# Performance work log

Hardware: AMD Instinct MI355X
Metric: run time of the kernel (lower is better)

The kernel has to match this reference:

```python
import jax, jax.numpy as jnp
import numpy as np

N_HEADS = 4
NS_STEPS = 5
NS_EPS = 1e-7

def newtonschulz5(G):
    # G: [out, in]; quintic Newton-Schulz, 5 steps. out==in here so no transpose branch needed,
    # but keep the static-shape check for faithfulness.
    a, b, c = 3.4445, -4.775, 2.0315
    X = G / (jnp.linalg.norm(G) + NS_EPS)
    transposed = G.shape[0] > G.shape[1]
    if transposed:
        X = X.T
    def step(X, _):
        A = X @ X.T
        B = b * A + c * (A @ A)
        return a * X + B @ X, None
    X, _ = jax.lax.scan(step, X, None, length=NS_STEPS)
    if transposed:
        X = X.T
    return X

def setup_inputs() -> dict:
    key = jax.random.key(0)
    k1, k2, k3, k4, k5 = jax.random.split(key, 5)
    B, S, D_in, D_out, r = 4, 2048, 4096, 4096, 16
    init_std = 0.01 / np.sqrt(D_out * r)
    return {
        "x": jax.random.normal(k1, (B, S, D_in), dtype=jnp.float32),
        "W": jax.random.normal(k2, (D_out, D_in), dtype=jnp.float32) * 0.02,
        "bias": jax.random.normal(k3, (D_out,), dtype=jnp.float32) * 0.02,
        "lora_A": jax.random.normal(k4, (r, D_in), dtype=jnp.float32),
        "lora_B": jax.random.normal(k5, (D_out, r), dtype=jnp.float32) * init_std,
    }

def reference(x, W, bias, lora_A, lora_B):
    # base linear (frozen weights); dropout is identity (p=0 / eval)
    base_out = jnp.einsum('bsi,oi->bso', x, W) + bias
    r, D_in = lora_A.shape
    D_out = lora_B.shape[0]
    hr = r // N_HEADS
    Ah = lora_A.reshape(N_HEADS, hr, D_in)                       # [h, hr, in]
    Bh = lora_B.reshape(D_out, N_HEADS, hr).transpose(1, 0, 2)    # [h, out, hr]
    G = jnp.einsum('hor,hri->hoi', Bh, Ah)                        # [h, out, in]
    alpha = jnp.sqrt(jnp.sum(G * G, axis=(1, 2)))                 # per-head Frobenius norm
    M = jax.vmap(newtonschulz5)(G)                                # [h, out, in]
    lora_out = jnp.einsum('h,hoi,bsi->bso', alpha, M, x)
    return base_out + lora_out
```

## Files before the change

### kernel.cpp

```cpp
#include <hip/hip_runtime.h>
#include <math.h>

#define MDIM 8192
#define NDIM 4096
#define KDIM 4096

typedef __attribute__((ext_vector_type(8))) _Float16 h8;
typedef __attribute__((ext_vector_type(4))) _Float16 h4;
typedef __attribute__((ext_vector_type(4))) float f32x4;

typedef const __attribute__((address_space(1))) void* gas_ptr;
typedef __attribute__((address_space(3))) void* las_ptr;

__device__ inline void load16_to_lds(const void* g, void* l) {
  __builtin_amdgcn_global_load_lds((gas_ptr)g, (las_ptr)l, 16, 0, 0);
}

__device__ inline void mm4(const double* A, const double* B, double* C) {
#pragma unroll
  for (int p = 0; p < 4; ++p)
#pragma unroll
    for (int q = 0; q < 4; ++q) {
      double s = 0.0;
#pragma unroll
      for (int r = 0; r < 4; ++r) s += A[p * 4 + r] * B[r * 4 + q];
      C[p * 4 + q] = s;
    }
}
__device__ inline void mm4_bt(const double* A, const double* B, double* C) {
#pragma unroll
  for (int p = 0; p < 4; ++p)
#pragma unroll
    for (int q = 0; q < 4; ++q) {
      double s = 0.0;
#pragma unroll
      for (int r = 0; r < 4; ++r) s += A[p * 4 + r] * B[q * 4 + r];
      C[p * 4 + q] = s;
    }
}

__global__ void ns_kernel(const float* __restrict__ lora_A,
                          const float* __restrict__ lora_B,
                          float* __restrict__ E) {
  const int h = blockIdx.x;
  const int tid = threadIdx.x;
  const int lane = tid & 63;
  const int wave = tid >> 6;

  float gu[16], gv[16];
#pragma unroll
  for (int e = 0; e < 16; ++e) { gu[e] = 0.f; gv[e] = 0.f; }

  for (int o = tid; o < NDIM; o += 256) {
    const float4 bv = *(const float4*)(lora_B + (size_t)o * 16 + h * 4);
    const float bb[4] = {bv.x, bv.y, bv.z, bv.w};
#pragma unroll
    for (int p = 0; p < 4; ++p)
#pragma unroll
      for (int q = 0; q < 4; ++q) gu[p * 4 + q] += bb[p] * bb[q];
  }
  for (int i = tid; i < KDIM; i += 256) {
    float aa[4];
#pragma unroll
    for (int p = 0; p < 4; ++p) aa[p] = lora_A[(size_t)(h * 4 + p) * KDIM + i];
#pragma unroll
    for (int p = 0; p < 4; ++p)
#pragma unroll
      for (int q = 0; q < 4; ++q) gv[p * 4 + q] += aa[p] * aa[q];
  }

#pragma unroll
  for (int e = 0; e < 16; ++e) {
#pragma unroll
    for (int off = 32; off > 0; off >>= 1) {
      gu[e] += __shfl_down(gu[e], off, 64);
      gv[e] += __shfl_down(gv[e], off, 64);
    }
  }
  __shared__ float pu[4][16], pv[4][16];
  if (lane == 0) {
#pragma unroll
    for (int e = 0; e < 16; ++e) { pu[wave][e] = gu[e]; pv[wave][e] = gv[e]; }
  }
  __syncthreads();

  if (tid == 0) {
    double gud[16], gvd[16];
#pragma unroll
    for (int e = 0; e < 16; ++e) {
      gud[e] = (double)pu[0][e] + pu[1][e] + pu[2][e] + pu[3][e];
      gvd[e] = (double)pv[0][e] + pv[1][e] + pv[2][e] + pv[3][e];
    }
    double tr = 0.0;
#pragma unroll
    for (int e = 0; e < 16; ++e) tr += gud[e] * gvd[e];
    const double alpha = sqrt(tr);
    const double n0 = alpha + 1e-7;

    double C[16] = {0};
    C[0] = C[5] = C[10] = C[15] = 1.0 / n0;

    const double a = 3.4445, b = -4.775, c = 2.0315;
    for (int it = 0; it < 5; ++it) {
      double T1[16], D[16], DG[16], DGD[16], GuC[16], F[16], Cn[16];
      mm4(C, gvd, T1);
      mm4_bt(T1, C, D);
      mm4(D, gud, DG);
      mm4(DG, D, DGD);
      mm4(gud, C, GuC);
#pragma unroll
      for (int e = 0; e < 16; ++e) F[e] = b * D[e] + c * DGD[e];
      mm4(F, GuC, Cn);
#pragma unroll
      for (int e = 0; e < 16; ++e) C[e] = a * C[e] + Cn[e];
    }
#pragma unroll
    for (int e = 0; e < 16; ++e) E[h * 16 + e] = (float)(alpha * C[e]);
  }
}

__global__ void weff_kernel(const float* __restrict__ W,
                            const float* __restrict__ lora_A,
                            const float* __restrict__ lora_B,
                            const float* __restrict__ E,
                            _Float16* __restrict__ Wh) {
  const int tid = threadIdx.x;
  __shared__ float cf[16][16];
  __shared__ __align__(16) float Asm[16][1024];
  const int o0 = (blockIdx.x >> 1) * 16;
  const int kh = (blockIdx.x & 1) * 2048;
  {
    const int r = tid >> 4, kk = tid & 15, h = kk >> 2, q = kk & 3;
    float s = 0.f;
#pragma unroll
    for (int p = 0; p < 4; ++p)
      s += lora_B[(size_t)(o0 + r) * 16 + h * 4 + p] * E[h * 16 + p * 4 + q];
    cf[r][kk] = s;
  }
  for (int kb = kh; kb < kh + 2048; kb += 1024) {
    __syncthreads();
#pragma unroll
    for (int j = 0; j < 16; ++j) {
      const int f4 = tid + j * 256;
      const int k = f4 >> 8, c4 = f4 & 255;
      *(float4*)&Asm[k][c4 * 4] =
          *(const float4*)&lora_A[(size_t)k * KDIM + kb + (size_t)c4 * 4];
    }
    __syncthreads();
    float4 av[16];
#pragma unroll
    for (int k = 0; k < 16; ++k) av[k] = *(const float4*)&Asm[k][tid * 4];
#pragma unroll
    for (int r = 0; r < 16; ++r) {
      const size_t base = (size_t)(o0 + r) * KDIM + kb + tid * 4;
      float4 acc = *(const float4*)&W[base];
#pragma unroll
      for (int k = 0; k < 16; ++k) {
        const float cfv = cf[r][k];
        acc.x += cfv * av[k].x; acc.y += cfv * av[k].y;
        acc.z += cfv * av[k].z; acc.w += cfv * av[k].w;
      }
      h4 pk;
      pk[0] = (_Float16)acc.x; pk[1] = (_Float16)acc.y;
      pk[2] = (_Float16)acc.z; pk[3] = (_Float16)acc.w;
      *(h4*)(Wh + base) = pk;
    }
  }
}

__global__ void xcast_kernel(const float* __restrict__ x,
                             _Float16* __restrict__ Xh) {
  const size_t t = (size_t)blockIdx.x * 256 + threadIdx.x;
  const size_t base = t * 8;
  const float4 a = *(const float4*)(x + base);
  const float4 b = *(const float4*)(x + base + 4);
  h8 o;
  o[0] = (_Float16)a.x; o[1] = (_Float16)a.y; o[2] = (_Float16)a.z; o[3] = (_Float16)a.w;
  o[4] = (_Float16)b.x; o[5] = (_Float16)b.y; o[6] = (_Float16)b.z; o[7] = (_Float16)b.w;
  *(h8*)(Xh + base) = o;
}

__launch_bounds__(512, 2)
__global__ void gemm_kernel(const _Float16* __restrict__ Xh,
                            const _Float16* __restrict__ Wh,
                            const float* __restrict__ bias,
                            float* __restrict__ out) {
  __shared__ __align__(16) _Float16 sA0_0[128 * 64], sA0_1[128 * 64];
  __shared__ __align__(16) _Float16 sA1_0[128 * 64], sA1_1[128 * 64];
  __shared__ __align__(16) _Float16 sB0_0[128 * 64], sB0_1[128 * 64];
  __shared__ __align__(16) _Float16 sB1_0[128 * 64], sB1_1[128 * 64];

  const int tid = threadIdx.x;
  const int lane = tid & 63;
  const int wave = tid >> 6;
  const int wm = wave >> 2;
  const int wn = wave & 3;
  const int quad = lane >> 4;
  const int r16 = lane & 15;
  const int sw = r16 & 7;

  const int lin = blockIdx.x;
  const int wg = (lin & 7) * 64 + (lin >> 3);
  const int bm = wg >> 4;
  const int bn = wg & 15;

  const int row0 = tid >> 3;
  const int lc0 = (tid & 7) ^ (row0 & 7);
  const size_t off0 = (size_t)row0 * KDIM + lc0 * 8;
  const int ldsb = tid * 16;
  const _Float16* pA0 = Xh + (size_t)(bm * 256) * KDIM;
  const _Float16* pA1 = pA0 + (size_t)128 * KDIM;
  const _Float16* pB0 = Wh + (size_t)(bn * 256) * KDIM;
  const _Float16* pB1 = pB0 + (size_t)128 * KDIM;

  const int aRow = (wm * 64 + r16) * 64;
  const int bRow = (wn * 32 + r16) * 64;
  const int c0 = (quad ^ sw) * 8;
  const int c1 = ((quad + 4) ^ sw) * 8;

  f32x4 acc[2][2][4][2] = {};
  h8 a0[4][2], a1[4][2], b0[2][2], b1[2][2];

#define STAGE(arr, p, koff) do {                                               \
    load16_to_lds((p) + off0 + (koff), (char*)(arr) + ldsb);                   \
    load16_to_lds((p) + off0 + (size_t)64 * KDIM + (koff),                     \
                  (char*)(arr) + ldsb + 8192);                                 \
  } while (0)

#define FENCE() asm volatile("" ::: "memory")
#define BAR() do { FENCE(); __builtin_amdgcn_s_barrier(); FENCE(); } while (0)
#define VMC(n) asm volatile("s_waitcnt vmcnt(" #n ")" ::: "memory")

#define RDA(dst, Aarr) do { _Pragma("unroll")                                  \
    for (int f = 0; f < 4; ++f) {                                              \
      dst[f][0] = *(const h8*)&Aarr[aRow + f * 1024 + c0];                     \
      dst[f][1] = *(const h8*)&Aarr[aRow + f * 1024 + c1];                     \
    } } while (0)
#define RDB(dst, Barr) do { _Pragma("unroll")                                  \
    for (int g = 0; g < 2; ++g) {                                              \
      dst[g][0] = *(const h8*)&Barr[bRow + g * 1024 + c0];                     \
      dst[g][1] = *(const h8*)&Barr[bRow + g * 1024 + c1];                     \
    } } while (0)

#define MFMA16(MQ, NQ, AV, BV) do {                                            \
    __builtin_amdgcn_s_setprio(1);                                             \
    _Pragma("unroll")                                                          \
    for (int f = 0; f < 4; ++f)                                                \
      _Pragma("unroll")                                                        \
      for (int g = 0; g < 2; ++g) {                                            \
        acc[MQ][NQ][f][g] = __builtin_amdgcn_mfma_f32_16x16x32_f16(            \
            AV[f][0], BV[g][0], acc[MQ][NQ][f][g], 0, 0, 0);                   \
        acc[MQ][NQ][f][g] = __builtin_amdgcn_mfma_f32_16x16x32_f16(            \
            AV[f][1], BV[g][1], acc[MQ][NQ][f][g], 0, 0, 0);                   \
      }                                                                        \
    __builtin_amdgcn_s_setprio(0);                                             \
  } while (0)

#define NOP() do { } while (0)

#define PH(RDS, STG, MQ, NQ, AV, BV, VMW) do {                                 \
    RDS;                                                                       \
    STG;                                                                       \
    BAR();                                                                     \
    MFMA16(MQ, NQ, AV, BV);                                                    \
    VMW;                                                                       \
    BAR();                                                                     \
  } while (0)

#define TILE_EVEN(t) do {                                                      \
    PH({ RDA(a0, sA0_0); RDB(b0, sB0_0); },                                    \
       STAGE(sA0_1, pA0, ((t) + 1) * 64), 0, 0, a0, b0, VMC(6));               \
    PH(RDA(a1, sA1_0), STAGE(sB1_1, pB1, ((t) + 1) * 64), 1, 0, a1, b0, VMC(6)); \
    PH(RDB(b1, sB1_0), STAGE(sB0_0, pB0, ((t) + 2) * 64), 1, 1, a1, b1, VMC(6)); \
    PH(NOP(),          STAGE(sA1_0, pA1, ((t) + 2) * 64), 0, 1, a0, b1, VMC(6)); \
  } while (0)

#define TILE_ODD(t) do {                                                       \
    PH({ RDA(a0, sA0_1); RDB(b0, sB0_1); },                                    \
       STAGE(sA0_0, pA0, ((t) + 1) * 64), 0, 0, a0, b0, VMC(6));               \
    PH(RDA(a1, sA1_1), STAGE(sB1_0, pB1, ((t) + 1) * 64), 1, 0, a1, b0, VMC(6)); \
    PH(RDB(b1, sB1_1), STAGE(sB0_1, pB0, ((t) + 2) * 64), 1, 1, a1, b1, VMC(6)); \
    PH(NOP(),          STAGE(sA1_1, pA1, ((t) + 2) * 64), 0, 1, a0, b1, VMC(6)); \
  } while (0)

#define TILE_62() do {                                                         \
    PH({ RDA(a0, sA0_0); RDB(b0, sB0_0); },                                    \
       STAGE(sA0_1, pA0, 63 * 64), 0, 0, a0, b0, VMC(6));                      \
    PH(RDA(a1, sA1_0), STAGE(sB1_1, pB1, 63 * 64), 1, 0, a1, b0, VMC(6));      \
    PH(RDB(b1, sB1_0), NOP(), 1, 1, a1, b1, VMC(4));                           \
    PH(NOP(),          NOP(), 0, 1, a0, b1, VMC(2));                           \
  } while (0)

#define TILE_63() do {                                                         \
    PH({ RDA(a0, sA0_1); RDB(b0, sB0_1); }, NOP(), 0, 0, a0, b0, VMC(0));      \
    PH(RDA(a1, sA1_1), NOP(), 1, 0, a1, b0, NOP());                            \
    PH(RDB(b1, sB1_1), NOP(), 1, 1, a1, b1, NOP());                            \
    PH(NOP(),          NOP(), 0, 1, a0, b1, NOP());                            \
  } while (0)

  STAGE(sB0_0, pB0, 0);
  STAGE(sA1_0, pA1, 0);
  STAGE(sA0_0, pA0, 0);
  STAGE(sB1_0, pB1, 0);
  STAGE(sB0_1, pB0, 64);
  STAGE(sA1_1, pA1, 64);
  VMC(4);
  BAR();

#pragma unroll 1
  for (int t2 = 0; t2 < 62; t2 += 2) {
    TILE_EVEN(t2);
    TILE_ODD(t2 + 1);
  }
  TILE_62();
  TILE_63();

#pragma unroll
  for (int mq = 0; mq < 2; ++mq)
#pragma unroll
    for (int f = 0; f < 4; ++f) {
      float* po = out + (size_t)(bm * 256 + mq * 128 + wm * 64 + f * 16 + quad * 4) * NDIM;
#pragma unroll
      for (int nq = 0; nq < 2; ++nq)
#pragma unroll
        for (int g = 0; g < 2; ++g) {
          const int ocol = bn * 256 + nq * 128 + wn * 32 + g * 16 + r16;
          const float bb = bias[ocol];
          const f32x4 v = acc[mq][nq][f][g];
#pragma unroll
          for (int rg = 0; rg < 4; ++rg)
            po[(size_t)rg * NDIM + ocol] = v[rg] + bb;
        }
    }
}

extern "C" void kernel_launch(void* const* d_in, const int* in_sizes, int n_in,
                              void* d_out, int out_size, void* d_ws, size_t ws_size,
                              hipStream_t stream) {
  const float* x      = (const float*)d_in[0];
  const float* W      = (const float*)d_in[1];
  const float* bias   = (const float*)d_in[2];
  const float* lora_A = (const float*)d_in[3];
  const float* lora_B = (const float*)d_in[4];
  float* out = (float*)d_out;

  char* ws = (char*)d_ws;
  float* E = (float*)ws;
  _Float16* Wh = (_Float16*)(ws + 1024);
  _Float16* Xh = (_Float16*)(ws + 1024 + (size_t)NDIM * KDIM * 2);

  ns_kernel<<<dim3(4), dim3(256), 0, stream>>>(lora_A, lora_B, E);
  xcast_kernel<<<dim3((MDIM * KDIM) / (256 * 8)), dim3(256), 0, stream>>>(x, Xh);
  weff_kernel<<<dim3(512), dim3(256), 0, stream>>>(W, lora_A, lora_B, E, Wh);
  gemm_kernel<<<dim3(512), dim3(512), 0, stream>>>(Xh, Wh, bias, out);
}
```

Before: 583.5 us.

## Restructure GEMM to 256x128 tiles with 4 waves and triple-buffered K=32 stages

Replaces the 256x256 block tile with 8 waves and double buffering at K=64 by a 256x128 tile with 4 waves. The K loop now steps by 32 through a three-deep LDS ring. Each wave computes a 128x64 sub-tile with a larger register accumulator, and the grid doubles to 1024 blocks. The goal is more pipeline depth and better per-wave operand reuse. The cost is lower arithmetic intensity per block, more global traffic, and more barriers per unit of work.

```diff
diff --git a/kernel.cpp b/kernel.cpp
--- a/kernel.cpp
+++ b/kernel.cpp
@@ -180,157 +180,125 @@
   *(h8*)(Xh + base) = o;
 }
 
-__launch_bounds__(512, 2)
+__launch_bounds__(256, 2)
 __global__ void gemm_kernel(const _Float16* __restrict__ Xh,
                             const _Float16* __restrict__ Wh,
                             const float* __restrict__ bias,
                             float* __restrict__ out) {
-  __shared__ __align__(16) _Float16 sA0_0[128 * 64], sA0_1[128 * 64];
-  __shared__ __align__(16) _Float16 sA1_0[128 * 64], sA1_1[128 * 64];
-  __shared__ __align__(16) _Float16 sB0_0[128 * 64], sB0_1[128 * 64];
-  __shared__ __align__(16) _Float16 sB1_0[128 * 64], sB1_1[128 * 64];
+  __shared__ __align__(16) _Float16 A0s[256 * 32], A1s[256 * 32], A2s[256 * 32];
+  __shared__ __align__(16) _Float16 B0s[128 * 32], B1s[128 * 32], B2s[128 * 32];
 
   const int tid = threadIdx.x;
   const int lane = tid & 63;
   const int wave = tid >> 6;
-  const int wm = wave >> 2;
-  const int wn = wave & 3;
+  const int wm = wave >> 1;
+  const int wn = wave & 1;
   const int quad = lane >> 4;
   const int r16 = lane & 15;
-  const int sw = r16 & 7;
+  const int swk = (r16 >> 1) & 3;
 
   const int lin = blockIdx.x;
-  const int wg = (lin & 7) * 64 + (lin >> 3);
-  const int bm = wg >> 4;
-  const int bn = wg & 15;
-
-  const int row0 = tid >> 3;
-  const int lc0 = (tid & 7) ^ (row0 & 7);
-  const size_t off0 = (size_t)row0 * KDIM + lc0 * 8;
+  const int wg = (lin & 7) * 128 + (lin >> 3);
+  const int bm = wg >> 5;
+  const int bn = wg & 31;
+
+  const int srow = tid >> 2;
+  const int slc = (tid & 3) ^ ((srow >> 1) & 3);
+  const size_t soff = (size_t)srow * KDIM + slc * 8;
   const int ldsb = tid * 16;
-  const _Float16* pA0 = Xh + (size_t)(bm * 256) * KDIM;
-  const _Float16* pA1 = pA0 + (size_t)128 * KDIM;
-  const _Float16* pB0 = Wh + (size_t)(bn * 256) * KDIM;
-  const _Float16* pB1 = pB0 + (size_t)128 * KDIM;
-
-  const int aRow = (wm * 64 + r16) * 64;
-  const int bRow = (wn * 32 + r16) * 64;
-  const int c0 = (quad ^ sw) * 8;
-  const int c1 = ((quad + 4) ^ sw) * 8;
-
-  f32x4 acc[2][2][4][2] = {};
-  h8 a0[4][2], a1[4][2], b0[2][2], b1[2][2];
-
-#define STAGE(arr, p, koff) do {                                               \
-    load16_to_lds((p) + off0 + (koff), (char*)(arr) + ldsb);                   \
-    load16_to_lds((p) + off0 + (size_t)64 * KDIM + (koff),                     \
-                  (char*)(arr) + ldsb + 8192);                                 \
-  } while (0)
+  const _Float16* pA = Xh + (size_t)(bm * 256) * KDIM;
+  const _Float16* pB = Wh + (size_t)(bn * 128) * KDIM;
+
+  const int aBase = (wm * 128 + r16) * 32;
+  const int bBase = (wn * 64 + r16) * 32;
+  const int c0 = (quad ^ swk) * 8;
+
+  f32x4 acc[2][4][4] = {};
+  h8 a0[4], a1[4], bb[4];
 
 #define FENCE() asm volatile("" ::: "memory")
 #define BAR() do { FENCE(); __builtin_amdgcn_s_barrier(); FENCE(); } while (0)
 #define VMC(n) asm volatile("s_waitcnt vmcnt(" #n ")" ::: "memory")
-
-#define RDA(dst, Aarr) do { _Pragma("unroll")                                  \
-    for (int f = 0; f < 4; ++f) {                                              \
-      dst[f][0] = *(const h8*)&Aarr[aRow + f * 1024 + c0];                     \
-      dst[f][1] = *(const h8*)&Aarr[aRow + f * 1024 + c1];                     \
-    } } while (0)
-#define RDB(dst, Barr) do { _Pragma("unroll")                                  \
-    for (int g = 0; g < 2; ++g) {                                              \
-      dst[g][0] = *(const h8*)&Barr[bRow + g * 1024 + c0];                     \
-      dst[g][1] = *(const h8*)&Barr[bRow + g * 1024 + c1];                     \
-    } } while (0)
-
-#define MFMA16(MQ, NQ, AV, BV) do {                                            \
+#define NOPV() do { } while (0)
+
+#define RDA(dst, Ac, F0) do { _Pragma("unroll")                                \
+    for (int i = 0; i < 4; ++i)                                                \
+      dst[i] = *(const h8*)&Ac[aBase + ((F0) + i) * 512 + c0];                 \
+  } while (0)
+#define RDB(dst, Bc) do { _Pragma("unroll")                                    \
+    for (int g = 0; g < 4; ++g)                                                \
+      dst[g] = *(const h8*)&Bc[bBase + g * 512 + c0];                          \
+  } while (0)
+
+#define STG_A01(An, kn) do {                                                   \
+    load16_to_lds(pA + soff + (kn), (char*)(An) + ldsb);                       \
+    load16_to_lds(pA + soff + (size_t)64 * KDIM + (kn),                        \
+                  (char*)(An) + 4096 + ldsb);                                  \
+  } while (0)
+#define STG_A23B(An, Bn, kn) do {                                              \
+    load16_to_lds(pA + soff + (size_t)128 * KDIM + (kn),                       \
+                  (char*)(An) + 8192 + ldsb);                                  \
+    load16_to_lds(pA + soff + (size_t)192 * KDIM + (kn),                       \
+                  (char*)(An) + 12288 + ldsb);                                 \
+    load16_to_lds(pB + soff + (kn), (char*)(Bn) + ldsb);                       \
+    load16_to_lds(pB + soff + (size_t)64 * KDIM + (kn),                        \
+                  (char*)(Bn) + 4096 + ldsb);                                  \
+  } while (0)
+
+#define MFMA_H(H, AV) do {                                                     \
     __builtin_amdgcn_s_setprio(1);                                             \
     _Pragma("unroll")                                                          \
-    for (int f = 0; f < 4; ++f)                                                \
+    for (int i = 0; i < 4; ++i)                                                \
       _Pragma("unroll")                                                        \
-      for (int g = 0; g < 2; ++g) {                                            \
-        acc[MQ][NQ][f][g] = __builtin_amdgcn_mfma_f32_16x16x32_f16(            \
-            AV[f][0], BV[g][0], acc[MQ][NQ][f][g], 0, 0, 0);                   \
-        acc[MQ][NQ][f][g] = __builtin_amdgcn_mfma_f32_16x16x32_f16(            \
-            AV[f][1], BV[g][1], acc[MQ][NQ][f][g], 0, 0, 0);                   \
-      }                                                                        \
+      for (int g = 0; g < 4; ++g)                                              \
+        acc[H][i][g] = __builtin_amdgcn_mfma_f32_16x16x32_f16(                 \
+            AV[i], bb[g], acc[H][i][g], 0, 0, 0);                              \
     __builtin_amdgcn_s_setprio(0);                                             \
   } while (0)
 
-#define NOP() do { } while (0)
-
-#define PH(RDS, STG, MQ, NQ, AV, BV, VMW) do {                                 \
-    RDS;                                                                       \
-    STG;                                                                       \
-    BAR();                                                                     \
-    MFMA16(MQ, NQ, AV, BV);                                                    \
-    VMW;                                                                       \
-    BAR();                                                                     \
-  } while (0)
-
-#define TILE_EVEN(t) do {                                                      \
-    PH({ RDA(a0, sA0_0); RDB(b0, sB0_0); },                                    \
-       STAGE(sA0_1, pA0, ((t) + 1) * 64), 0, 0, a0, b0, VMC(6));               \
-    PH(RDA(a1, sA1_0), STAGE(sB1_1, pB1, ((t) + 1) * 64), 1, 0, a1, b0, VMC(6)); \
-    PH(RDB(b1, sB1_0), STAGE(sB0_0, pB0, ((t) + 2) * 64), 1, 1, a1, b1, VMC(6)); \
-    PH(NOP(),          STAGE(sA1_0, pA1, ((t) + 2) * 64), 0, 1, a0, b1, VMC(6)); \
-  } while (0)
-
-#define TILE_ODD(t) do {                                                       \
-    PH({ RDA(a0, sA0_1); RDB(b0, sB0_1); },                                    \
-       STAGE(sA0_0, pA0, ((t) + 1) * 64), 0, 0, a0, b0, VMC(6));               \
-    PH(RDA(a1, sA1_1), STAGE(sB1_0, pB1, ((t) + 1) * 64), 1, 0, a1, b0, VMC(6)); \
-    PH(RDB(b1, sB1_1), STAGE(sB0_1, pB0, ((t) + 2) * 64), 1, 1, a1, b1, VMC(6)); \
-    PH(NOP(),          STAGE(sA1_1, pA1, ((t) + 2) * 64), 0, 1, a0, b1, VMC(6)); \
-  } while (0)
-
-#define TILE_62() do {                                                         \
-    PH({ RDA(a0, sA0_0); RDB(b0, sB0_0); },                                    \
-       STAGE(sA0_1, pA0, 63 * 64), 0, 0, a0, b0, VMC(6));                      \
-    PH(RDA(a1, sA1_0), STAGE(sB1_1, pB1, 63 * 64), 1, 0, a1, b0, VMC(6));      \
-    PH(RDB(b1, sB1_0), NOP(), 1, 1, a1, b1, VMC(4));                           \
-    PH(NOP(),          NOP(), 0, 1, a0, b1, VMC(2));                           \
-  } while (0)
-
-#define TILE_63() do {                                                         \
-    PH({ RDA(a0, sA0_1); RDB(b0, sB0_1); }, NOP(), 0, 0, a0, b0, VMC(0));      \
-    PH(RDA(a1, sA1_1), NOP(), 1, 0, a1, b0, NOP());                            \
-    PH(RDB(b1, sB1_1), NOP(), 1, 1, a1, b1, NOP());                            \
-    PH(NOP(),          NOP(), 0, 1, a0, b1, NOP());                            \
-  } while (0)
-
-  STAGE(sB0_0, pB0, 0);
-  STAGE(sA1_0, pA1, 0);
-  STAGE(sA0_0, pA0, 0);
-  STAGE(sB1_0, pB1, 0);
-  STAGE(sB0_1, pB0, 64);
-  STAGE(sA1_1, pA1, 64);
-  VMC(4);
+#define STEP(Ac, Bc, An, Bn, kn) do {                                          \
+    RDA(a0, Ac, 0); RDB(bb, Bc); STG_A01(An, kn);                              \
+    BAR(); MFMA_H(0, a0); BAR();                                               \
+    RDA(a1, Ac, 4); STG_A23B(An, Bn, kn);                                      \
+    BAR(); MFMA_H(1, a1); VMC(6); BAR();                                       \
+  } while (0)
+
+#define STEP_TAIL(Ac, Bc, VEND) do {                                           \
+    RDA(a0, Ac, 0); RDB(bb, Bc);                                               \
+    BAR(); MFMA_H(0, a0); BAR();                                               \
+    RDA(a1, Ac, 4);                                                            \
+    BAR(); MFMA_H(1, a1); VEND; BAR();                                         \
+  } while (0)
+
+  STG_A01(A0s, 0);  STG_A23B(A0s, B0s, 0);
+  STG_A01(A1s, 32); STG_A23B(A1s, B1s, 32);
+  VMC(6);
   BAR();
 
 #pragma unroll 1
-  for (int t2 = 0; t2 < 62; t2 += 2) {
-    TILE_EVEN(t2);
-    TILE_ODD(t2 + 1);
-  }
-  TILE_62();
-  TILE_63();
-
-#pragma unroll
-  for (int mq = 0; mq < 2; ++mq)
-#pragma unroll
-    for (int f = 0; f < 4; ++f) {
-      float* po = out + (size_t)(bm * 256 + mq * 128 + wm * 64 + f * 16 + quad * 4) * NDIM;
-#pragma unroll
-      for (int nq = 0; nq < 2; ++nq)
-#pragma unroll
-        for (int g = 0; g < 2; ++g) {
-          const int ocol = bn * 256 + nq * 128 + wn * 32 + g * 16 + r16;
-          const float bb = bias[ocol];
-          const f32x4 v = acc[mq][nq][f][g];
-#pragma unroll
-          for (int rg = 0; rg < 4; ++rg)
-            po[(size_t)rg * NDIM + ocol] = v[rg] + bb;
-        }
+  for (int t = 0; t < 126; t += 3) {
+    STEP(A0s, B0s, A2s, B2s, (t + 2) * 32);
+    STEP(A1s, B1s, A0s, B0s, (t + 3) * 32);
+    STEP(A2s, B2s, A1s, B1s, (t + 4) * 32);
+  }
+  STEP_TAIL(A0s, B0s, VMC(0));
+  STEP_TAIL(A1s, B1s, NOPV());
+
+#pragma unroll
+  for (int h = 0; h < 2; ++h)
+#pragma unroll
+    for (int i = 0; i < 4; ++i) {
+      float* po = out +
+          (size_t)(bm * 256 + wm * 128 + (h * 4 + i) * 16 + quad * 4) * NDIM;
+#pragma unroll
+      for (int g = 0; g < 4; ++g) {
+        const int ocol = bn * 128 + wn * 64 + g * 16 + r16;
+        const float bv = bias[ocol];
+        const f32x4 v = acc[h][i][g];
+#pragma unroll
+        for (int rg = 0; rg < 4; ++rg)
+          po[(size_t)rg * NDIM + ocol] = v[rg] + bv;
+      }
     }
 }
 
@@ -352,5 +320,5 @@
   ns_kernel<<<dim3(4), dim3(256), 0, stream>>>(lora_A, lora_B, E);
   xcast_kernel<<<dim3((MDIM * KDIM) / (256 * 8)), dim3(256), 0, stream>>>(x, Xh);
   weff_kernel<<<dim3(512), dim3(256), 0, stream>>>(W, lora_A, lora_B, E, Wh);
-  gemm_kernel<<<dim3(512), dim3(512), 0, stream>>>(Xh, Wh, bias, out);
-}
+  gemm_kernel<<<dim3(1024), dim3(256), 0, stream>>>(Xh, Wh, bias, out);
+}
```

After: 636.7 us. +9.1%, slower.
